# Kernel optimization log

Measured on AMD Instinct MI355X. Metric: run time of the kernel, lower is better.

The kernel has to match this reference:

```python
import jax, jax.numpy as jnp
import numpy as np

NEG_INF = -1e9  # matches tf mask value -1000000000.0
LEAKY_ALPHA = 0.2  # tf.nn.leaky_relu default


def setup_inputs() -> dict:
    key = jax.random.key(0)
    k1, k2, k3, k4 = jax.random.split(key, 4)
    B, N, F, U = 8, 2048, 128, 128
    X = jax.random.normal(k1, (B, N, F), dtype=jnp.float32)
    A = jax.random.randint(k2, (B, N, N), 0, 2, dtype=jnp.int32)
    W = jax.random.normal(k3, (F, U), dtype=jnp.float32) * 0.1
    a = jax.random.normal(k4, (2 * U, 1), dtype=jnp.float32) * 0.1
    return {"X": X, "A": A, "W": W, "a": a}


def reference(X, A, W, a):
    # H = X @ W : [B, N, U]
    H = jnp.einsum('bnf,fu->bnu', X, W)
    U = H.shape[-1]
    # Additive decomposition of the tile+concat: [H_i || H_j] @ a = H_i@a_src + H_j@a_dst
    a_src = a[:U, 0]   # [U]
    a_dst = a[U:, 0]   # [U]
    s = H @ a_src      # [B, N]
    t = H @ a_dst      # [B, N]
    e = s[:, :, None] + t[:, None, :]            # [B, N, N] pairwise logits
    e = jax.nn.leaky_relu(e, negative_slope=LEAKY_ALPHA)
    mask = jnp.where(A > 0, 0.0, NEG_INF).astype(e.dtype)
    attention = jax.nn.softmax(e + mask, axis=-1)  # [B, N, N]
    H_out = jnp.einsum('bij,bju->biu', attention, H)
    return jax.nn.relu(H_out)
```

## Files before the change

### kernel.cpp

```cpp
#include <hip/hip_runtime.h>
#include <hip/hip_bf16.h>


#define NEG_INF -1.0e9f

typedef __bf16 bf16x8 __attribute__((ext_vector_type(8)));
typedef unsigned short ushort8 __attribute__((ext_vector_type(8)));
typedef float f32x4 __attribute__((ext_vector_type(4)));

__device__ __forceinline__ unsigned short f2b(float x) {
    unsigned u = __builtin_bit_cast(unsigned, x);
    u += 0x7fffu + ((u >> 16) & 1u);
    return (unsigned short)(u >> 16);
}

__device__ __forceinline__ void gload_lds16(const void* g, void* l) {
    __builtin_amdgcn_global_load_lds(
        (const __attribute__((address_space(1))) void*)g,
        (__attribute__((address_space(3))) void*)l, 16, 0, 0);
}

__global__ __launch_bounds__(256) void k_wt(const float* __restrict__ W,
                                            unsigned short* __restrict__ WT) {
    int tid = blockIdx.x * 256 + threadIdx.x;
    int u = tid >> 7, f = tid & 127;
    WT[tid] = f2b(W[f * 128 + u]);
}

__global__ __launch_bounds__(256) void k_h(const float* __restrict__ X,
                                           const unsigned short* __restrict__ WT,
                                           const float* __restrict__ a,
                                           unsigned short* __restrict__ HT,
                                           float* __restrict__ sbuf,
                                           float* __restrict__ tbuf) {
    const int tid  = threadIdx.x;
    const int w    = tid >> 6;
    const int lane = tid & 63;
    const int r    = lane & 15;
    const int cg   = lane >> 4;
    const int row0 = blockIdx.x * 64 + w * 16;
    const int b    = row0 >> 11;
    const int n0   = row0 & 2047;
    const int arow = row0 + r;

    f32x4 acc[8] = {};

#pragma unroll
    for (int k0 = 0; k0 < 128; k0 += 32) {
        const float* xp = X + (size_t)arow * 128 + k0 + cg * 8;
        ushort8 xa;
#pragma unroll
        for (int j = 0; j < 8; j++) xa[j] = f2b(xp[j]);
        bf16x8 av = __builtin_bit_cast(bf16x8, xa);
#pragma unroll
        for (int ut = 0; ut < 8; ut++) {
            ushort8 wb = *(const ushort8*)(WT + (size_t)(ut * 16 + r) * 128 + k0 + cg * 8);
            acc[ut] = __builtin_amdgcn_mfma_f32_16x16x32_bf16(
                av, __builtin_bit_cast(bf16x8, wb), acc[ut], 0, 0, 0);
        }
    }

    float sp[4] = {0.f, 0.f, 0.f, 0.f};
    float tp[4] = {0.f, 0.f, 0.f, 0.f};
#pragma unroll
    for (int ut = 0; ut < 8; ut++) {
        int u = ut * 16 + r;
        float as = a[u];
        float ad = a[128 + u];
#pragma unroll
        for (int reg = 0; reg < 4; reg++) {
            float h = acc[ut][reg];
            int nrow = n0 + cg * 4 + reg;
            HT[((size_t)b * 128 + u) * 2048 + nrow] = f2b(h);
            sp[reg] += h * as;
            tp[reg] += h * ad;
        }
    }
#pragma unroll
    for (int msk = 1; msk < 16; msk <<= 1) {
#pragma unroll
        for (int reg = 0; reg < 4; reg++) {
            sp[reg] += __shfl_xor(sp[reg], msk);
            tp[reg] += __shfl_xor(tp[reg], msk);
        }
    }
    if (r == 0) {
#pragma unroll
        for (int reg = 0; reg < 4; reg++) {
            int row = row0 + cg * 4 + reg;
            sbuf[row] = sp[reg];
            tbuf[row] = tp[reg];
        }
    }
}

__global__ __launch_bounds__(512, 4) void k_attn(const int* __restrict__ A,
                                                 const unsigned short* __restrict__ HT,
                                                 const float* __restrict__ sbuf,
                                                 const float* __restrict__ tbuf,
                                                 float* __restrict__ out) {
    __shared__ char smem[65536];
    __shared__ float dSm[4][2][16];

    const int tid  = threadIdx.x;
    const int w    = tid >> 6;
    const int lane = tid & 63;
    const int r    = lane & 15;
    const int cg   = lane >> 4;
    const int g    = w & 1;
    const int jq   = w >> 1;
    const int bid  = blockIdx.x;
    const int b    = bid & 7;
    const int it   = bid >> 3;
    const int i0   = it * 32;
    const int rot  = it & 15;

    const int irow = i0 + g * 16 + r;
    const float s_r   = sbuf[b * 2048 + irow];
    const int* Arow   = A + ((size_t)(b * 2048 + irow)) * 2048 + jq * 512;
    const float* trow = tbuf + b * 2048 + jq * 512;
    const unsigned short* Hb = HT + ((size_t)b * 128) * 2048 + jq * 512;

    const int srow = (lane >> 2);
    const int csrc = (lane & 3) ^ ((lane >> 2) & 3);
    char* const qbase = smem + jq * 16384;
    const unsigned short* src0 = Hb + (size_t)(g * 64 + srow) * 2048 + csrc * 8;

    f32x4 acc[8] = {};
    float den = 0.f;

    int4 cA0, cA1; float4 cT0, cT1;
    {
        const int j0 = rot * 32;
#pragma unroll
        for (int i = 0; i < 4; i++)
            gload_lds16(src0 + (size_t)i * 16 * 2048 + j0,
                        qbase + (g * 4 + i) * 1024);
        const int off = j0 + cg * 8;
        cA0 = *(const int4*)(Arow + off);
        cA1 = *(const int4*)(Arow + off + 4);
        cT0 = *(const float4*)(trow + off);
        cT1 = *(const float4*)(trow + off + 4);
    }
    __syncthreads();

    for (int k = 0; k < 16; ++k) {
        const int p = k & 1;
        int4 nA0, nA1; float4 nT0, nT1;
        if (k < 15) {
            const int j0n = ((k + 1 + rot) & 15) * 32;
            char* dst = qbase + (p ^ 1) * 8192;
#pragma unroll
            for (int i = 0; i < 4; i++)
                gload_lds16(src0 + (size_t)i * 16 * 2048 + j0n,
                            dst + (g * 4 + i) * 1024);
            const int off = j0n + cg * 8;
            nA0 = *(const int4*)(Arow + off);
            nA1 = *(const int4*)(Arow + off + 4);
            nT0 = *(const float4*)(trow + off);
            nT1 = *(const float4*)(trow + off + 4);
        }

        int   ai[8] = {cA0.x, cA0.y, cA0.z, cA0.w, cA1.x, cA1.y, cA1.z, cA1.w};
        float tv[8] = {cT0.x, cT0.y, cT0.z, cT0.w, cT1.x, cT1.y, cT1.z, cT1.w};
        bf16x8 pa;
#pragma unroll
        for (int jj = 0; jj < 8; jj++) {
            float x = s_r + tv[jj];
            float e = fmaxf(x, 0.2f * x);
            e = ai[jj] > 0 ? e : NEG_INF;
            float pp = __expf(e - 16.0f);
            den += pp;
            pa[jj] = (__bf16)pp;
        }

        const char* buf = qbase + p * 8192;
#pragma unroll
        for (int ut = 0; ut < 8; ut++) {
            ushort8 hb = *(const ushort8*)(buf + (ut * 16 + r) * 64 +
                                           ((cg ^ (r & 3)) * 16));
            acc[ut] = __builtin_amdgcn_mfma_f32_16x16x32_bf16(
                pa, __builtin_bit_cast(bf16x8, hb), acc[ut], 0, 0, 0);
        }

        if (k < 15) { cA0 = nA0; cA1 = nA1; cT0 = nT0; cT1 = nT1; }
        __syncthreads();
    }

    den += __shfl_xor(den, 16);
    den += __shfl_xor(den, 32);

    float* accS = (float*)smem;
    if (cg == 0) dSm[jq][g][r] = den;
    if (jq != 0) {
        const int rowIdx = ((jq - 1) * 2 + g) * 16 + cg * 4;
#pragma unroll
        for (int ut = 0; ut < 8; ut++)
#pragma unroll
            for (int reg = 0; reg < 4; reg++)
                accS[(rowIdx + reg) * 132 + ut * 16 + r] = acc[ut][reg];
    }
    __syncthreads();
    if (jq == 0) {
        float dinv[4];
#pragma unroll
        for (int reg = 0; reg < 4; reg++) {
            const int row = cg * 4 + reg;
            dinv[reg] = 1.0f / (dSm[0][g][row] + dSm[1][g][row] +
                                dSm[2][g][row] + dSm[3][g][row]);
        }
#pragma unroll
        for (int ut = 0; ut < 8; ut++) {
#pragma unroll
            for (int reg = 0; reg < 4; reg++) {
                const int lrow = cg * 4 + reg;
                float num = acc[ut][reg]
                          + accS[((0 * 2 + g) * 16 + lrow) * 132 + ut * 16 + r]
                          + accS[((1 * 2 + g) * 16 + lrow) * 132 + ut * 16 + r]
                          + accS[((2 * 2 + g) * 16 + lrow) * 132 + ut * 16 + r];
                float o = fmaxf(num * dinv[reg], 0.f);
                out[((size_t)(b * 2048 + i0 + g * 16 + lrow)) * 128 +
                    ut * 16 + r] = o;
            }
        }
    }
}

extern "C" void kernel_launch(void* const* d_in, const int* in_sizes, int n_in,
                              void* d_out, int out_size, void* d_ws, size_t ws_size,
                              hipStream_t stream) {
    const float* X = (const float*)d_in[0];
    const int*   A = (const int*)d_in[1];
    const float* W = (const float*)d_in[2];
    const float* a = (const float*)d_in[3];
    float* out = (float*)d_out;

    char* ws = (char*)d_ws;
    unsigned short* WT  = (unsigned short*)(ws);
    float*          sb  = (float*)(ws + 32768);
    float*          tb  = (float*)(ws + 32768 + 65536);
    unsigned short* HT  = (unsigned short*)(ws + 32768 + 131072);

    k_wt<<<dim3(64), dim3(256), 0, stream>>>(W, WT);
    k_h<<<dim3(256), dim3(256), 0, stream>>>(X, WT, a, HT, sb, tb);
    k_attn<<<dim3(512), dim3(512), 0, stream>>>(A, HT, sb, tb, out);
}
```

Measured before the change: 61.63 us.

## Pack adjacency mask to bits in H kernel and stage t in LDS

New measurement: 87.21 us. +41.5%, slower.

```diff
diff --git a/kernel.cpp b/kernel.cpp
--- a/kernel.cpp
+++ b/kernel.cpp
@@ -27,15 +27,29 @@
     WT[tid] = f2b(W[f * 128 + u]);
 }
 
-__global__ __launch_bounds__(256) void k_h(const float* __restrict__ X,
-                                           const unsigned short* __restrict__ WT,
-                                           const float* __restrict__ a,
-                                           unsigned short* __restrict__ HT,
-                                           float* __restrict__ sbuf,
-                                           float* __restrict__ tbuf) {
+__global__ __launch_bounds__(256) void k_h_pack(const float* __restrict__ X,
+                                                const unsigned short* __restrict__ WT,
+                                                const float* __restrict__ a,
+                                                const int* __restrict__ A,
+                                                unsigned short* __restrict__ HT,
+                                                float* __restrict__ sbuf,
+                                                float* __restrict__ tbuf,
+                                                unsigned int* __restrict__ Abits) {
     const int tid  = threadIdx.x;
     const int w    = tid >> 6;
     const int lane = tid & 63;
+
+    if (blockIdx.x >= 256) {
+        const int wid = (blockIdx.x - 256) * 4 + w;
+        for (int c = wid; c < 524288; c += 4096) {
+            int av = A[(size_t)c * 64 + lane];
+            unsigned long long m = __ballot(av > 0);
+            if (lane == 0)
+                *(unsigned long long*)(Abits + (size_t)c * 2) = m;
+        }
+        return;
+    }
+
     const int r    = lane & 15;
     const int cg   = lane >> 4;
     const int row0 = blockIdx.x * 64 + w * 16;
@@ -94,12 +108,13 @@
     }
 }
 
-__global__ __launch_bounds__(512, 4) void k_attn(const int* __restrict__ A,
+__global__ __launch_bounds__(512, 4) void k_attn(const unsigned int* __restrict__ Abits,
                                                  const unsigned short* __restrict__ HT,
                                                  const float* __restrict__ sbuf,
                                                  const float* __restrict__ tbuf,
                                                  float* __restrict__ out) {
     __shared__ char smem[65536];
+    __shared__ float tS[2048];
     __shared__ float dSm[4][2][16];
 
     const int tid  = threadIdx.x;
@@ -116,60 +131,56 @@
     const int rot  = it & 15;
 
     const int irow = i0 + g * 16 + r;
-    const float s_r   = sbuf[b * 2048 + irow];
-    const int* Arow   = A + ((size_t)(b * 2048 + irow)) * 2048 + jq * 512;
-    const float* trow = tbuf + b * 2048 + jq * 512;
+    const float s_r = sbuf[b * 2048 + irow];
+    const unsigned int* Mrow = Abits + ((size_t)(b * 2048 + irow)) * 64 + jq * 16;
     const unsigned short* Hb = HT + ((size_t)b * 128) * 2048 + jq * 512;
 
     const int srow = (lane >> 2);
-    const int csrc = (lane & 3) ^ ((lane >> 2) & 3);
+    const int csrc = (lane & 3) ^ ((lane >> 2) & 3) ^ ((lane >> 4) & 3);
     char* const qbase = smem + jq * 16384;
     const unsigned short* src0 = Hb + (size_t)(g * 64 + srow) * 2048 + csrc * 8;
+    const int rsl = ((r & 3) ^ ((r >> 2) & 3));
 
     f32x4 acc[8] = {};
     float den = 0.f;
 
-    int4 cA0, cA1; float4 cT0, cT1;
+    *(float4*)(tS + tid * 4) = *(const float4*)(tbuf + b * 2048 + tid * 4);
+
+    unsigned int mw = Mrow[rot];
     {
         const int j0 = rot * 32;
 #pragma unroll
         for (int i = 0; i < 4; i++)
             gload_lds16(src0 + (size_t)i * 16 * 2048 + j0,
                         qbase + (g * 4 + i) * 1024);
-        const int off = j0 + cg * 8;
-        cA0 = *(const int4*)(Arow + off);
-        cA1 = *(const int4*)(Arow + off + 4);
-        cT0 = *(const float4*)(trow + off);
-        cT1 = *(const float4*)(trow + off + 4);
     }
     __syncthreads();
 
     for (int k = 0; k < 16; ++k) {
         const int p = k & 1;
-        int4 nA0, nA1; float4 nT0, nT1;
+        unsigned int mwn = 0;
         if (k < 15) {
-            const int j0n = ((k + 1 + rot) & 15) * 32;
+            const int kn = (k + 1 + rot) & 15;
             char* dst = qbase + (p ^ 1) * 8192;
 #pragma unroll
             for (int i = 0; i < 4; i++)
-                gload_lds16(src0 + (size_t)i * 16 * 2048 + j0n,
+                gload_lds16(src0 + (size_t)i * 16 * 2048 + kn * 32,
                             dst + (g * 4 + i) * 1024);
-            const int off = j0n + cg * 8;
-            nA0 = *(const int4*)(Arow + off);
-            nA1 = *(const int4*)(Arow + off + 4);
-            nT0 = *(const float4*)(trow + off);
-            nT1 = *(const float4*)(trow + off + 4);
-        }
-
-        int   ai[8] = {cA0.x, cA0.y, cA0.z, cA0.w, cA1.x, cA1.y, cA1.z, cA1.w};
-        float tv[8] = {cT0.x, cT0.y, cT0.z, cT0.w, cT1.x, cT1.y, cT1.z, cT1.w};
+            mwn = Mrow[kn];
+        }
+
+        const float* tq = tS + jq * 512 + ((k + rot) & 15) * 32 + cg * 8;
+        float4 t0 = *(const float4*)(tq);
+        float4 t1 = *(const float4*)(tq + 4);
+        float tv[8] = {t0.x, t0.y, t0.z, t0.w, t1.x, t1.y, t1.z, t1.w};
+        const unsigned int sh = mw >> (cg * 8);
         bf16x8 pa;
 #pragma unroll
         for (int jj = 0; jj < 8; jj++) {
             float x = s_r + tv[jj];
             float e = fmaxf(x, 0.2f * x);
-            e = ai[jj] > 0 ? e : NEG_INF;
             float pp = __expf(e - 16.0f);
+            pp = ((sh >> jj) & 1u) ? pp : 0.f;
             den += pp;
             pa[jj] = (__bf16)pp;
         }
@@ -178,12 +189,12 @@
 #pragma unroll
         for (int ut = 0; ut < 8; ut++) {
             ushort8 hb = *(const ushort8*)(buf + (ut * 16 + r) * 64 +
-                                           ((cg ^ (r & 3)) * 16));
+                                           ((cg ^ rsl) * 16));
             acc[ut] = __builtin_amdgcn_mfma_f32_16x16x32_bf16(
                 pa, __builtin_bit_cast(bf16x8, hb), acc[ut], 0, 0, 0);
         }
 
-        if (k < 15) { cA0 = nA0; cA1 = nA1; cT0 = nT0; cT1 = nT1; }
+        mw = mwn;
         __syncthreads();
     }
 
@@ -238,10 +249,11 @@
     char* ws = (char*)d_ws;
     unsigned short* WT  = (unsigned short*)(ws);
     float*          sb  = (float*)(ws + 32768);
-    float*          tb  = (float*)(ws + 32768 + 65536);
-    unsigned short* HT  = (unsigned short*)(ws + 32768 + 131072);
+    float*          tb  = (float*)(ws + 98304);
+    unsigned short* HT  = (unsigned short*)(ws + 163840);
+    unsigned int*   Ab  = (unsigned int*)(ws + 163840 + 4194304);
 
     k_wt<<<dim3(64), dim3(256), 0, stream>>>(W, WT);
-    k_h<<<dim3(256), dim3(256), 0, stream>>>(X, WT, a, HT, sb, tb);
-    k_attn<<<dim3(512), dim3(512), 0, stream>>>(A, HT, sb, tb, out);
-}
+    k_h_pack<<<dim3(1280), dim3(256), 0, stream>>>(X, WT, a, A, HT, sb, tb, Ab);
+    k_attn<<<dim3(512), dim3(512), 0, stream>>>(Ab, HT, sb, tb, out);
+}
```
